# Performance work log

Measured on AMD Instinct MI355X. Metric: run time of the kernel, lower is better.

Reference implementation:

```python
import jax, jax.numpy as jnp
from jax import lax
import numpy as np

PROB_SIZE = 512  # m = n = prob_size
QP_ITERS = 20    # fixed-iteration differentiable projected-gradient QP solve (CvxpyLayer surrogate)


def setup_inputs() -> dict:
    key = jax.random.key(0)
    ks = jax.random.split(key, 4)
    b, p, d = 16, PROB_SIZE, 128
    mk = lambda k: jax.random.normal(k, (b, p, d), dtype=jnp.float32) * 0.05
    return {
        "n_emb_cur": mk(ks[0]),
        "e_emb_cur": mk(ks[1]),
        "n_emb_nxt": mk(ks[2]),
        "e_emb_nxt": mk(ks[3]),
    }


def _pairwise_sqdist(a, b):
    # Kpp_x1 + Kpp_x2 - 2*Kpp_g from the torch code: ||a_i||^2 + ||b_j||^2 - 2 a_i.b_j
    g = jnp.einsum('bid,bjd->bij', a, b)            # (b, m, n) Gram
    da = jnp.sum(a * a, axis=-1)[:, :, None]        # diag(a a^T) broadcast over j
    db = jnp.sum(b * b, axis=-1)[:, None, :]        # diag(b b^T) broadcast over i
    return da + db - 2.0 * g


def _get_Q(n_emb_cur, e_emb_cur, n_emb_nxt, e_emb_nxt):
    Kp = _pairwise_sqdist(n_emb_cur, n_emb_nxt)     # (b, m, n) node kernel
    Kq = _pairwise_sqdist(e_emb_cur, e_emb_nxt)     # (b, m, n) edge kernel
    bsz, m, n = Kp.shape
    # torch: Kp.transpose(1,2).reshape(b,-1)  -> n-major flattening (x[j*m+i])
    q = 0.5 * (Kp + Kq).transpose(0, 2, 1).reshape(bsz, n * m)
    return q


def _qp_solve(q, m, n, iters=QP_ITERS):
    # Fixed-iteration projected gradient descent, differentiable and jit-able.
    bsz = q.shape[0]
    qm = q.reshape(bsz, n, m)
    X0 = jnp.full((bsz, n, m), 1.0 / m, dtype=q.dtype)  # feasible init
    lr = 0.5 / (jnp.sum(qm * qm, axis=(1, 2), keepdims=True) + 1e-8)

    def step(X, _):
        s = jnp.sum(qm * X, axis=(1, 2), keepdims=True)   # q.x
        X = X - lr * (2.0 * s * qm)                        # gradient of (q.x)^2
        X = jnp.clip(X, 0.0, 1.0)                          # box constraint
        X = X / (jnp.sum(X, axis=2, keepdims=True) + 1e-8) # equality: row sums = 1
        col = jnp.sum(X, axis=1, keepdims=True)
        X = X * jnp.minimum(1.0, 2.0 / (col + 1e-8))       # inequality: col sums <= 2
        return X, None

    X, _ = lax.scan(step, X0, None, length=iters)
    return X.reshape(bsz, n * m)


def reference(n_emb_cur, e_emb_cur, n_emb_nxt, e_emb_nxt):
    m = n = PROB_SIZE
    q = _get_Q(n_emb_cur, e_emb_cur, n_emb_nxt, e_emb_nxt)  # (b, m*n) cost vector
    x_star = _qp_solve(q, m, n)                              # (b, m*n)
    return x_star
```

## Files before the change

kernel.cpp:

```cpp
#include <hip/hip_runtime.h>

#define BATCH 16
#define NN 512
#define MM 512
#define DD 128
#define QP_ITERS 20
#define NBLK (BATCH * 16)
#define SLOT 1024
#define PSZ ((size_t)BATCH * 512 * DD)

typedef __attribute__((ext_vector_type(8))) short bf16x8;
typedef __attribute__((ext_vector_type(4))) float f32x4;

#define LDR 56

__device__ __forceinline__ unsigned short bf16_rne(float f) {
    unsigned u = __float_as_uint(f);
    return (unsigned short)((u + 0x7FFFu + ((u >> 16) & 1u)) >> 16);
}

__device__ __forceinline__ void split4(float4 v, uint2& hi, uint2& lo) {
    unsigned short h0 = bf16_rne(v.x), h1 = bf16_rne(v.y),
                   h2 = bf16_rne(v.z), h3 = bf16_rne(v.w);
    hi.x = (unsigned)h0 | ((unsigned)h1 << 16);
    hi.y = (unsigned)h2 | ((unsigned)h3 << 16);
    unsigned short l0 = bf16_rne(v.x - __uint_as_float((unsigned)h0 << 16));
    unsigned short l1 = bf16_rne(v.y - __uint_as_float((unsigned)h1 << 16));
    unsigned short l2 = bf16_rne(v.z - __uint_as_float((unsigned)h2 << 16));
    unsigned short l3 = bf16_rne(v.w - __uint_as_float((unsigned)h3 << 16));
    lo.x = (unsigned)l0 | ((unsigned)l1 << 16);
    lo.y = (unsigned)l2 | ((unsigned)l3 << 16);
}

__device__ __forceinline__ float dot4(float4 v) {
    return v.x*v.x + v.y*v.y + v.z*v.z + v.w*v.w;
}

__global__ __launch_bounds__(256, 4) void convert_kernel(
    const float* __restrict__ s0, const float* __restrict__ s1,
    unsigned short* __restrict__ h0p, unsigned short* __restrict__ l0p,
    unsigned short* __restrict__ h1p, unsigned short* __restrict__ l1p,
    float* __restrict__ nrm)
{
    int tid  = threadIdx.x;
    int lane = tid & 63;
    int w    = tid >> 6;
    int half = lane >> 5;
    int c4   = (lane & 31) * 4;
    int row  = blockIdx.x * 8 + w * 2 + half;
    size_t off = (size_t)row * DD + c4;

    float4 v0 = *(const float4*)(s0 + off);
    float4 v1 = *(const float4*)(s1 + off);
    uint2 h, l;
    split4(v0, h, l);
    *(uint2*)&h0p[off] = h;  *(uint2*)&l0p[off] = l;
    split4(v1, h, l);
    *(uint2*)&h1p[off] = h;  *(uint2*)&l1p[off] = l;

    float ns = dot4(v0) + dot4(v1);
    #pragma unroll
    for (int m = 1; m <= 16; m <<= 1) ns += __shfl_xor(ns, m);
    if ((lane & 31) == 0) nrm[row] = ns;
}

__global__ __launch_bounds__(256, 2) void gemm_q_kernel(
    const unsigned short* __restrict__ pl,
    const float* __restrict__ rcur, const float* __restrict__ rnxt,
    float* __restrict__ qm, float* __restrict__ qsums,
    float* __restrict__ q2sums, unsigned* __restrict__ flags)
{
    int b  = blockIdx.z;
    int it = blockIdx.x;
    int jt = blockIdx.y;
    int tid = threadIdx.x;

    if (it == 0 && jt == 0 && b == 0) {
        flags[tid] = 0u; flags[tid + 256] = 0u;
    }

    __shared__ __align__(16) unsigned short sAh[64 * LDR];
    __shared__ __align__(16) unsigned short sAl[64 * LDR];
    __shared__ __align__(16) unsigned short sBh[128 * LDR];
    __shared__ __align__(16) unsigned short sBl[128 * LDR];

    int l  = tid & 63;
    int wv = tid >> 6;
    int wi = wv & 1;
    int wj = wv >> 1;
    int lm = l & 15;
    int lg = l >> 4;

    int ar = tid >> 2, ak = (tid & 3) * 8;
    int br = tid >> 1, bk = (tid & 1) * 16;

    size_t abase = ((size_t)b*NN + jt*64)  * DD;
    size_t bbase = ((size_t)b*MM + it*128) * DD;
    const unsigned short* aH[2] = { pl + 0*PSZ + abase, pl + 2*PSZ + abase };
    const unsigned short* aL[2] = { pl + 1*PSZ + abase, pl + 3*PSZ + abase };
    const unsigned short* bH[2] = { pl + 4*PSZ + bbase, pl + 6*PSZ + bbase };
    const unsigned short* bL[2] = { pl + 5*PSZ + bbase, pl + 7*PSZ + bbase };

    f32x4 acc[2][4];
    #pragma unroll
    for (int a = 0; a < 2; ++a)
        #pragma unroll
        for (int c = 0; c < 4; ++c) acc[a][c] = (f32x4){0.f, 0.f, 0.f, 0.f};

    for (int s = 0; s < 8; ++s) {
        int mt = s >> 2, kb = (s & 3) * 32;
        size_t ao = (size_t)ar * DD + kb + ak;
        size_t bo = (size_t)br * DD + kb + bk;
        uint4 vah  = *(const uint4*)(aH[mt] + ao);
        uint4 val  = *(const uint4*)(aL[mt] + ao);
        uint4 vbh0 = *(const uint4*)(bH[mt] + bo);
        uint4 vbh1 = *(const uint4*)(bH[mt] + bo + 8);
        uint4 vbl0 = *(const uint4*)(bL[mt] + bo);
        uint4 vbl1 = *(const uint4*)(bL[mt] + bo + 8);

        __syncthreads();
        *(uint4*)&sAh[ar*LDR + ak]     = vah;
        *(uint4*)&sAl[ar*LDR + ak]     = val;
        *(uint4*)&sBh[br*LDR + bk]     = vbh0;
        *(uint4*)&sBh[br*LDR + bk + 8] = vbh1;
        *(uint4*)&sBl[br*LDR + bk]     = vbl0;
        *(uint4*)&sBl[br*LDR + bk + 8] = vbl1;
        __syncthreads();

        bf16x8 ah[2], al[2];
        #pragma unroll
        for (int jf = 0; jf < 2; ++jf) {
            int rr = wj*32 + jf*16 + lm;
            ah[jf] = *(const bf16x8*)&sAh[rr*LDR + lg*8];
            al[jf] = *(const bf16x8*)&sAl[rr*LDR + lg*8];
        }
        #pragma unroll
        for (int ff = 0; ff < 4; ++ff) {
            int rr = wi*64 + ff*16 + lm;
            bf16x8 bh = *(const bf16x8*)&sBh[rr*LDR + lg*8];
            bf16x8 bl = *(const bf16x8*)&sBl[rr*LDR + lg*8];
            #pragma unroll
            for (int jf = 0; jf < 2; ++jf) {
                acc[jf][ff] = __builtin_amdgcn_mfma_f32_16x16x32_bf16(
                                  ah[jf], bh, acc[jf][ff], 0, 0, 0);
                acc[jf][ff] = __builtin_amdgcn_mfma_f32_16x16x32_bf16(
                                  ah[jf], bl, acc[jf][ff], 0, 0, 0);
                acc[jf][ff] = __builtin_amdgcn_mfma_f32_16x16x32_bf16(
                                  al[jf], bh, acc[jf][ff], 0, 0, 0);
            }
        }
    }

    float rci[4];
    #pragma unroll
    for (int ff = 0; ff < 4; ++ff)
        rci[ff] = rcur[(size_t)b*MM + it*128 + wi*64 + ff*16 + lm];

    float qs = 0.f, q2s = 0.f;
    #pragma unroll
    for (int jf = 0; jf < 2; ++jf) {
        #pragma unroll
        for (int r = 0; r < 4; ++r) {
            int j_loc = wj*32 + jf*16 + lg*4 + r;
            float rnj = rnxt[(size_t)b*NN + jt*64 + j_loc];
            size_t rowp = ((size_t)b*NN + jt*64 + j_loc) * MM + it*128;
            #pragma unroll
            for (int ff = 0; ff < 4; ++ff) {
                float v = 0.5f * (rci[ff] + rnj) - acc[jf][ff][r];
                qm[rowp + wi*64 + ff*16 + lm] = v;
                qs += v; q2s += v * v;
            }
        }
    }

    #pragma unroll
    for (int off = 32; off; off >>= 1) {
        qs  += __shfl_down(qs,  off);
        q2s += __shfl_down(q2s, off);
    }
    __shared__ float red[8];
    int lane = tid & 63;
    if (lane == 0) { red[wv] = qs; red[4 + wv] = q2s; }
    __syncthreads();
    if (tid == 0) {
        int tile = b * 32 + jt * 4 + it;
        qsums[tile]  = red[0] + red[1] + red[2] + red[3];
        q2sums[tile] = red[4] + red[5] + red[6] + red[7];
    }
}

__device__ __forceinline__ float gather16_sum_agent(const float* p)
{
    float acc = 0.f;
    #pragma unroll
    for (int g2 = 0; g2 < 16; ++g2)
        acc += __hip_atomic_load((float*)(p + g2 * SLOT), __ATOMIC_RELAXED,
                                 __HIP_MEMORY_SCOPE_AGENT);
    return acc;
}

__global__ __launch_bounds__(1024, 4) void qp_iter_kernel(
    const float* __restrict__ qm, const float* __restrict__ qsums,
    const float* __restrict__ q2sums, float* __restrict__ part,
    unsigned* __restrict__ flags, float* __restrict__ out)
{
    __shared__ float lds[16384 + 32];
    __shared__ int sh_ok;
    float* stage = lds;
    float* wred  = lds + 16384;

    int tid   = threadIdx.x;
    int blk   = blockIdx.x;
    int b     = blk >> 4;
    int g     = blk & 15;
    int w     = tid >> 6;
    int lane  = tid & 63;
    int r_loc = tid >> 5;
    int cseg  = tid & 31;
    int j     = g * 32 + r_loc;

    size_t rowbase = ((size_t)b * NN + j) * MM;

    if (w == 0) {
        float v1 = (lane < 32) ? qsums[b * 32 + lane]  : 0.f;
        float v2 = (lane < 32) ? q2sums[b * 32 + lane] : 0.f;
        #pragma unroll
        for (int m = 32; m; m >>= 1) {
            v1 += __shfl_xor(v1, m);
            v2 += __shfl_xor(v2, m);
        }
        if (lane == 0) { wred[0] = v1; wred[1] = v2; }
    }

    float q[16], x[16], fk[16];
    #pragma unroll
    for (int k = 0; k < 16; ++k) q[k] = qm[rowbase + cseg + 32*k];

    const float inv_m = 1.0f / (float)MM;
    #pragma unroll
    for (int k = 0; k < 16; ++k) { x[k] = inv_m; fk[k] = 1.0f; }

    __syncthreads();
    const float lr = 0.5f / (wred[1] + 1e-8f);
    float s = wred[0] * inv_m;

    unsigned* myflag = flags + b * 32 + g;
    unsigned* bflags = flags + b * 32;

    for (int t = 1; t <= QP_ITERS; ++t) {
        if (t > 1) {
            unsigned tt = (unsigned)(t - 1);
            if (w == 0) {
                unsigned v = (lane < 16)
                    ? __hip_atomic_load(bflags + lane, __ATOMIC_RELAXED,
                                        __HIP_MEMORY_SCOPE_AGENT)
                    : tt;
                int ok = __all(v >= tt);
                if (lane == 0) sh_ok = ok;
            }
            __syncthreads();

            const float* p = part + (size_t)((t - 1) & 1) * (NBLK * SLOT)
                           + (size_t)b * (16 * SLOT) + tid;
            float acc = gather16_sum_agent(p);

            if (!sh_ok) {
                if (w == 0) {
                    for (;;) {
                        unsigned v = (lane < 16)
                            ? __hip_atomic_load(bflags + lane, __ATOMIC_RELAXED,
                                                __HIP_MEMORY_SCOPE_AGENT)
                            : tt;
                        if (__all(v >= tt)) break;
                    }
                }
                __syncthreads();
                acc = gather16_sum_agent(p);
            }

            if (tid < 512) stage[tid] = fminf(1.0f, 2.0f / (acc + 1e-8f));
            else           stage[tid] = acc;
            __syncthreads();
            float v = (tid < 512) ? stage[tid] * stage[512 + tid] : 0.f;
            #pragma unroll
            for (int m = 32; m; m >>= 1) v += __shfl_xor(v, m);
            if (lane == 0) wred[w] = v;
            #pragma unroll
            for (int k = 0; k < 16; ++k) fk[k] = stage[cseg + 32*k];
            __syncthreads();
            float sacc = 0.f;
            #pragma unroll
            for (int i = 0; i < 16; ++i) sacc += wred[i];
            s = sacc;
        }

        float c = 2.0f * lr * s;
        float rp = 0.f;
        #pragma unroll
        for (int k = 0; k < 16; ++k) {
            float v = x[k] * fk[k] - c * q[k];
            v = fminf(fmaxf(v, 0.f), 1.f);
            x[k] = v;
            rp += v;
        }
        #pragma unroll
        for (int m = 16; m; m >>= 1) rp += __shfl_xor(rp, m);
        float inv = 1.0f / (rp + 1e-8f);
        #pragma unroll
        for (int k = 0; k < 16; ++k) x[k] *= inv;

        #pragma unroll
        for (int k = 0; k < 16; ++k) {
            float qx = q[k] * x[k];
            float px = x[k] + __shfl_xor(x[k], 32);
            float pq = qx   + __shfl_xor(qx,   32);
            int col = cseg + 32*k;
            if (lane < 32) lds[w * 512 + col]        = px;
            else           lds[8192 + w * 512 + col] = pq;
        }
        __syncthreads();
        {
            int arr = tid >> 9;
            int col = tid & 511;
            const float* basep = lds + arr * 8192 + col;
            float acc = 0.f;
            #pragma unroll
            for (int w2 = 0; w2 < 16; ++w2) acc += basep[w2 * 512];
            float* dst = part + (size_t)(t & 1) * (NBLK * SLOT)
                       + (size_t)blk * SLOT + tid;
            __hip_atomic_store(dst, acc, __ATOMIC_RELAXED,
                               __HIP_MEMORY_SCOPE_AGENT);
        }

        __syncthreads();
        if (tid == 0)
            __hip_atomic_store(myflag, (unsigned)t, __ATOMIC_RELEASE,
                               __HIP_MEMORY_SCOPE_AGENT);
    }

    {
        unsigned tt = (unsigned)QP_ITERS;
        if (w == 0) {
            for (;;) {
                unsigned v = (lane < 16)
                    ? __hip_atomic_load(bflags + lane, __ATOMIC_RELAXED,
                                        __HIP_MEMORY_SCOPE_AGENT)
                    : tt;
                if (__all(v >= tt)) break;
            }
        }
        __syncthreads();
        const float* p = part + (size_t)(QP_ITERS & 1) * (NBLK * SLOT)
                       + (size_t)b * (16 * SLOT) + tid;
        if (tid < 512) {
            float acc = gather16_sum_agent(p);
            stage[tid] = fminf(1.0f, 2.0f / (acc + 1e-8f));
        }
        __syncthreads();
        #pragma unroll
        for (int k = 0; k < 16; ++k)
            out[rowbase + cseg + 32*k] = x[k] * stage[cseg + 32*k];
    }
}

extern "C" void kernel_launch(void* const* d_in, const int* in_sizes, int n_in,
                              void* d_out, int out_size, void* d_ws, size_t ws_size,
                              hipStream_t stream)
{
    const float* nc = (const float*)d_in[0];
    const float* ec = (const float*)d_in[1];
    const float* nn = (const float*)d_in[2];
    const float* en = (const float*)d_in[3];
    float* out = (float*)d_out;

    float* ws = (float*)d_ws;
    const size_t QM_FLOATS = (size_t)BATCH * NN * MM;

    float* qm   = ws;
    float* part = ws + QM_FLOATS;
    float* qsums  = part + (size_t)2 * NBLK * SLOT;
    float* q2sums = qsums + 512;
    unsigned* flags = (unsigned*)(q2sums + 512);
    unsigned short* planes = (unsigned short*)(flags + 512);
    float* rcur = (float*)(planes + 8 * PSZ);
    float* rnxt = rcur + 8192;

    convert_kernel<<<dim3(1024), 256, 0, stream>>>(
        nn, en,
        planes + 0*PSZ, planes + 1*PSZ, planes + 2*PSZ, planes + 3*PSZ, rnxt);
    convert_kernel<<<dim3(1024), 256, 0, stream>>>(
        nc, ec,
        planes + 4*PSZ, planes + 5*PSZ, planes + 6*PSZ, planes + 7*PSZ, rcur);

    gemm_q_kernel<<<dim3(4, 8, BATCH), 256, 0, stream>>>(
        planes, rcur, rnxt, qm, qsums, q2sums, flags);

    qp_iter_kernel<<<dim3(NBLK), dim3(1024), 0, stream>>>(
        qm, qsums, q2sums, part, flags, out);
}
```

Before: 252.2 us.

## Merge convert launches and make every wave poll flags to cut block barriers

The two convert kernel launches are merged into a single 2048-block launch that chooses its source and plane pointers from the block index, which removes one launch. In the QP iteration kernel every wavefront now spins on the per-batch flags itself instead of relying on wave 0 plus a barrier and a speculative re-gather. Each wave also computes the full 512-element dot product redundantly rather than doing a cross-wave LDS reduction with an extra __syncthreads. The stage buffer is moved so it no longer overlaps the partial-sum staging area, which is needed once the barrier that used to separate them is gone. The cost is 16x more flag polling traffic and redundant reduction work per block.

```diff
diff --git a/kernel.cpp b/kernel.cpp
--- a/kernel.cpp
+++ b/kernel.cpp
@@ -37,17 +37,27 @@
 }
 
 __global__ __launch_bounds__(256, 4) void convert_kernel(
-    const float* __restrict__ s0, const float* __restrict__ s1,
-    unsigned short* __restrict__ h0p, unsigned short* __restrict__ l0p,
-    unsigned short* __restrict__ h1p, unsigned short* __restrict__ l1p,
-    float* __restrict__ nrm)
-{
+    const float* __restrict__ nc, const float* __restrict__ ec,
+    const float* __restrict__ nn, const float* __restrict__ en,
+    unsigned short* __restrict__ planes,
+    float* __restrict__ rcur, float* __restrict__ rnxt)
+{
+    int blk  = blockIdx.x;
+    int isCur = blk >> 10;
+    const float* s0 = isCur ? nc : nn;
+    const float* s1 = isCur ? ec : en;
+    unsigned short* h0p = planes + (size_t)(isCur ? 4 : 0) * PSZ;
+    unsigned short* l0p = h0p + PSZ;
+    unsigned short* h1p = h0p + 2 * PSZ;
+    unsigned short* l1p = h0p + 3 * PSZ;
+    float* nrm = isCur ? rcur : rnxt;
+
     int tid  = threadIdx.x;
     int lane = tid & 63;
     int w    = tid >> 6;
     int half = lane >> 5;
     int c4   = (lane & 31) * 4;
-    int row  = blockIdx.x * 8 + w * 2 + half;
+    int row  = (blk & 1023) * 8 + w * 2 + half;
     size_t off = (size_t)row * DD + c4;
 
     float4 v0 = *(const float4*)(s0 + off);
@@ -204,10 +214,9 @@
     const float* __restrict__ q2sums, float* __restrict__ part,
     unsigned* __restrict__ flags, float* __restrict__ out)
 {
-    __shared__ float lds[16384 + 32];
-    __shared__ int sh_ok;
-    float* stage = lds;
-    float* wred  = lds + 16384;
+    __shared__ float lds[16384 + 1024 + 16];
+    float* stage = lds + 16384;
+    float* wred  = lds + 16384 + 1024;
 
     int tid   = threadIdx.x;
     int blk   = blockIdx.x;
@@ -250,48 +259,33 @@
     for (int t = 1; t <= QP_ITERS; ++t) {
         if (t > 1) {
             unsigned tt = (unsigned)(t - 1);
-            if (w == 0) {
+            for (;;) {
                 unsigned v = (lane < 16)
                     ? __hip_atomic_load(bflags + lane, __ATOMIC_RELAXED,
                                         __HIP_MEMORY_SCOPE_AGENT)
                     : tt;
-                int ok = __all(v >= tt);
-                if (lane == 0) sh_ok = ok;
+                if (__all(v >= tt)) break;
             }
-            __syncthreads();
 
             const float* p = part + (size_t)((t - 1) & 1) * (NBLK * SLOT)
                            + (size_t)b * (16 * SLOT) + tid;
             float acc = gather16_sum_agent(p);
 
-            if (!sh_ok) {
-                if (w == 0) {
-                    for (;;) {
-                        unsigned v = (lane < 16)
-                            ? __hip_atomic_load(bflags + lane, __ATOMIC_RELAXED,
-                                                __HIP_MEMORY_SCOPE_AGENT)
-                            : tt;
-                        if (__all(v >= tt)) break;
-                    }
-                }
-                __syncthreads();
-                acc = gather16_sum_agent(p);
-            }
-
             if (tid < 512) stage[tid] = fminf(1.0f, 2.0f / (acc + 1e-8f));
             else           stage[tid] = acc;
             __syncthreads();
-            float v = (tid < 512) ? stage[tid] * stage[512 + tid] : 0.f;
+
+            float v = 0.f;
+            #pragma unroll
+            for (int kk = 0; kk < 8; ++kk) {
+                int c = lane + 64 * kk;
+                v += stage[c] * stage[512 + c];
+            }
             #pragma unroll
             for (int m = 32; m; m >>= 1) v += __shfl_xor(v, m);
-            if (lane == 0) wred[w] = v;
+            s = v;
             #pragma unroll
             for (int k = 0; k < 16; ++k) fk[k] = stage[cseg + 32*k];
-            __syncthreads();
-            float sacc = 0.f;
-            #pragma unroll
-            for (int i = 0; i < 16; ++i) sacc += wred[i];
-            s = sacc;
         }
 
         float c = 2.0f * lr * s;
@@ -340,16 +334,13 @@
 
     {
         unsigned tt = (unsigned)QP_ITERS;
-        if (w == 0) {
-            for (;;) {
-                unsigned v = (lane < 16)
-                    ? __hip_atomic_load(bflags + lane, __ATOMIC_RELAXED,
-                                        __HIP_MEMORY_SCOPE_AGENT)
-                    : tt;
-                if (__all(v >= tt)) break;
-            }
-        }
-        __syncthreads();
+        for (;;) {
+            unsigned v = (lane < 16)
+                ? __hip_atomic_load(bflags + lane, __ATOMIC_RELAXED,
+                                    __HIP_MEMORY_SCOPE_AGENT)
+                : tt;
+            if (__all(v >= tt)) break;
+        }
         const float* p = part + (size_t)(QP_ITERS & 1) * (NBLK * SLOT)
                        + (size_t)b * (16 * SLOT) + tid;
         if (tid < 512) {
@@ -385,12 +376,8 @@
     float* rcur = (float*)(planes + 8 * PSZ);
     float* rnxt = rcur + 8192;
 
-    convert_kernel<<<dim3(1024), 256, 0, stream>>>(
-        nn, en,
-        planes + 0*PSZ, planes + 1*PSZ, planes + 2*PSZ, planes + 3*PSZ, rnxt);
-    convert_kernel<<<dim3(1024), 256, 0, stream>>>(
-        nc, ec,
-        planes + 4*PSZ, planes + 5*PSZ, planes + 6*PSZ, planes + 7*PSZ, rcur);
+    convert_kernel<<<dim3(2048), 256, 0, stream>>>(
+        nc, ec, nn, en, planes, rcur, rnxt);
 
     gemm_q_kernel<<<dim3(4, 8, BATCH), 256, 0, stream>>>(
         planes, rcur, rnxt, qm, qsums, q2sums, flags);
```

Result: slower. 288.9 us (+14.6%).
